# Optimization experiments

Hardware: AMD Instinct MI355X
Metric: run time of the kernel (lower is better)

## Reference

```python
import jax, jax.numpy as jnp
import numpy as np

B, R, DIM = 4096, 64, 128


def setup_inputs() -> dict:
    key = jax.random.key(0)
    ks = jax.random.split(key, 8)
    return {
        "query_emb": jax.random.normal(ks[0], (B, DIM), jnp.float32),
        "offset_emb": jax.random.normal(ks[1], (B, DIM), jnp.float32),
        "refer_embs": jax.random.normal(ks[2], (B, R, DIM), jnp.float32),
        "query_r": jax.random.normal(ks[3], (B, DIM), jnp.float32),
        "refer_r": jax.random.normal(ks[4], (B, R, DIM), jnp.float32),
        "start_embs": jax.random.normal(ks[5], (B, R, DIM), jnp.float32),
        # attn_layer_1: Linear(2*dim, dim); xavier-uniform-like scale
        "W1": jax.random.uniform(ks[6], (DIM, 2 * DIM), jnp.float32, -0.125, 0.125),
        "b1": jnp.zeros((DIM,), jnp.float32),
        # attn_layer_2: Linear(dim, dim)
        "W2": jax.random.uniform(ks[7], (DIM, DIM), jnp.float32, -0.125, 0.125),
        "b2": jnp.zeros((DIM,), jnp.float32),
    }


def reference(query_emb, offset_emb, refer_embs, query_r, refer_r, start_embs, W1, b1, W2, b2):
    # bias term per neighbor: [B, R, dim]
    bias = refer_embs - (start_embs + refer_r)
    # concat([refer_r, broadcast(query_r)]) @ W1.T split to avoid materializing the concat:
    # W1 = [W1_a | W1_b] over the 2*dim input axis
    W1a, W1b = W1[:, :DIM], W1[:, DIM:]
    h = jnp.einsum('brd,kd->brk', refer_r, W1a) \
        + jnp.einsum('bd,kd->bk', query_r, W1b)[:, None, :] + b1
    h = jax.nn.relu(h)  # [B, R, dim]
    attn = jnp.einsum('brk,dk->brd', h, W2) + b2  # attn_layer_2
    final_refer_emb = jnp.sum(attn * bias, axis=-2)  # [B, dim]
    final_query_emb = query_emb + final_refer_emb
    return (final_query_emb, offset_emb)
```

## Files before the change

### kernel.cpp

```cpp
#include <hip/hip_runtime.h>
#include <hip/hip_bf16.h>
#include <stdint.h>

#define BTOT 4096
#define RR   64
#define DIMD 128

typedef short s16x8 __attribute__((ext_vector_type(8)));
typedef float f32x4 __attribute__((ext_vector_type(4)));

__device__ __forceinline__ unsigned short f2bf(float x) {
  __hip_bfloat16 h = __float2bfloat16(x);
  return __builtin_bit_cast(unsigned short, h);
}
__device__ __forceinline__ float bf2f(unsigned short u) {
  unsigned int v = ((unsigned int)u) << 16;
  return __builtin_bit_cast(float, v);
}

__global__ __launch_bounds__(256) void prep_kernel(
    const float* __restrict__ W1, const float* __restrict__ b1,
    const float* __restrict__ query_r, const float* __restrict__ W2,
    const float* __restrict__ offset_emb,
    float* __restrict__ qproj, unsigned short* __restrict__ w1a_swz,
    unsigned short* __restrict__ w2_swz, float* __restrict__ out)
{
  __shared__ float w1b[128 * 132];
  __shared__ float qrs[256];
  const int tid = threadIdx.x;

  {
    const size_t ob = (size_t)blockIdx.x * 8 * DIMD + (size_t)tid * 4;
    *reinterpret_cast<float4*>(out + (size_t)BTOT * DIMD + ob) =
        *reinterpret_cast<const float4*>(offset_emb + ob);
  }
  {
    const int k = tid >> 1, d0 = (tid & 1) * 64;
    const float* src = W1 + k * 256 + 128 + d0;
    float* dst = &w1b[k * 132 + d0];
    #pragma unroll
    for (int i = 0; i < 64; i += 4)
      *reinterpret_cast<float4*>(dst + i) = *reinterpret_cast<const float4*>(src + i);
  }
  if (blockIdx.x < 2) {
    const float* Wsrc = (blockIdx.x == 0) ? W1 : W2;
    unsigned short* dstw = (blockIdx.x == 0) ? w1a_swz : w2_swz;
    const int stride = (blockIdx.x == 0) ? 256 : 128;
    for (int i = tid; i < 128 * 128; i += 256) {
      const int k = i >> 7, d = i & 127;
      dstw[k * 128 + (d ^ ((k & 7) << 3))] = f2bf(Wsrc[k * stride + d]);
    }
  }
  __syncthreads();

  const int b0 = blockIdx.x * 8;
  const int k = tid & 127, bh = tid >> 7;
  for (int p = 0; p < 4; ++p) {
    const int b = b0 + p * 2;
    qrs[tid] = query_r[(size_t)(b + bh) * DIMD + k];
    __syncthreads();
    float acc = b1[k];
    const float* qq = &qrs[bh * 128];
    const float* wr = &w1b[k * 132];
    #pragma unroll
    for (int d = 0; d < 128; d += 4) {
      float4 wv = *reinterpret_cast<const float4*>(wr + d);
      float4 qv = *reinterpret_cast<const float4*>(qq + d);
      acc = fmaf(wv.x, qv.x, acc); acc = fmaf(wv.y, qv.y, acc);
      acc = fmaf(wv.z, qv.z, acc); acc = fmaf(wv.w, qv.w, acc);
    }
    qproj[(size_t)(b + bh) * DIMD + k] = acc;
    __syncthreads();
  }
}

__global__ __launch_bounds__(512) void main_kernel(
    const float* __restrict__ query_emb,
    const float* __restrict__ refer_embs, const float* __restrict__ refer_r,
    const float* __restrict__ start_embs, const float* __restrict__ b2,
    const float* __restrict__ qproj, const unsigned short* __restrict__ w1a_swz,
    const unsigned short* __restrict__ w2_swz, float* __restrict__ out)
{
  __shared__ unsigned short lds_w1a[128 * 128];
  __shared__ unsigned short lds_w2[128 * 128];
  __shared__ unsigned short wbuf[8][16 * 64];

  const int tid  = threadIdx.x;
  const int wave = tid >> 6;
  const int lane = tid & 63;
  const int g    = lane >> 4;
  const int c    = lane & 15;

  {
    const uint4* s1 = reinterpret_cast<const uint4*>(w1a_swz);
    const uint4* s2 = reinterpret_cast<const uint4*>(w2_swz);
    uint4* d1 = reinterpret_cast<uint4*>(lds_w1a);
    uint4* d2 = reinterpret_cast<uint4*>(lds_w2);
    #pragma unroll
    for (int i = 0; i < 4; ++i) {
      d1[tid + 512 * i] = s1[tid + 512 * i];
      d2[tid + 512 * i] = s2[tid + 512 * i];
    }
  }
  __syncthreads();

  unsigned short* mybuf = &wbuf[wave][0];
  const int srl  = lane >> 2;
  const int q    = lane & 3;
  const int sw_s = (srl & 7) << 3;
  const int swc  = (c & 7) << 3;
  const int rl4  = 4 * g;

  const int b = blockIdx.x * 8 + wave;

  float qn[8], b2v[8], acc[8];
  #pragma unroll
  for (int nt = 0; nt < 8; ++nt) {
    qn[nt]  = qproj[(size_t)b * DIMD + nt * 16 + c];
    b2v[nt] = b2[nt * 16 + c];
    acc[nt] = 0.f;
  }

  for (int it = 0; it < 4; ++it) {
    const size_t rowbase = ((size_t)b * RR + it * 16 + srl) * DIMD;
    uint4 bp[4];
    f32x4 Ch[8];
    #pragma unroll
    for (int nt = 0; nt < 8; ++nt) Ch[nt] = (f32x4){qn[nt], qn[nt], qn[nt], qn[nt]};

    #pragma unroll
    for (int H = 0; H < 2; ++H) {
      const size_t gb = rowbase + H * 64 + q * 16;
      float4 rv[4], ev[4], sv[4];
      #pragma unroll
      for (int i = 0; i < 4; ++i) {
        rv[i] = *reinterpret_cast<const float4*>(refer_r    + gb + 4 * i);
        ev[i] = *reinterpret_cast<const float4*>(refer_embs + gb + 4 * i);
        sv[i] = *reinterpret_cast<const float4*>(start_embs + gb + 4 * i);
      }
      {
        unsigned short* wrow = &mybuf[srl * 64];
        #pragma unroll
        for (int gi = 0; gi < 2; ++gi) {
          union { unsigned short u[8]; uint4 v; } pk;
          const float4 a = rv[2 * gi], bq = rv[2 * gi + 1];
          pk.u[0] = f2bf(a.x);  pk.u[1] = f2bf(a.y);
          pk.u[2] = f2bf(a.z);  pk.u[3] = f2bf(a.w);
          pk.u[4] = f2bf(bq.x); pk.u[5] = f2bf(bq.y);
          pk.u[6] = f2bf(bq.z); pk.u[7] = f2bf(bq.w);
          *reinterpret_cast<uint4*>(&wrow[(q * 16 + gi * 8) ^ sw_s]) = pk.v;
        }
      }
      #pragma unroll
      for (int gi = 0; gi < 2; ++gi) {
        union { unsigned short u[8]; uint4 v; } pk;
        const float4 e0 = ev[2 * gi], s0 = sv[2 * gi], f0 = rv[2 * gi];
        const float4 e1 = ev[2 * gi + 1], s1 = sv[2 * gi + 1], f1 = rv[2 * gi + 1];
        pk.u[0] = f2bf(e0.x - s0.x - f0.x); pk.u[1] = f2bf(e0.y - s0.y - f0.y);
        pk.u[2] = f2bf(e0.z - s0.z - f0.z); pk.u[3] = f2bf(e0.w - s0.w - f0.w);
        pk.u[4] = f2bf(e1.x - s1.x - f1.x); pk.u[5] = f2bf(e1.y - s1.y - f1.y);
        pk.u[6] = f2bf(e1.z - s1.z - f1.z); pk.u[7] = f2bf(e1.w - s1.w - f1.w);
        bp[2 * H + gi] = pk.v;
      }
      asm volatile("s_waitcnt lgkmcnt(0)" ::: "memory");
      s16x8 af0 = *reinterpret_cast<const s16x8*>(&mybuf[c * 64 + ((g * 8) ^ swc)]);
      s16x8 af1 = *reinterpret_cast<const s16x8*>(&mybuf[c * 64 + ((32 + g * 8) ^ swc)]);
      #pragma unroll
      for (int ks2 = 0; ks2 < 2; ++ks2)
        #pragma unroll
        for (int nt = 0; nt < 8; ++nt) {
          s16x8 wf = *reinterpret_cast<const s16x8*>(
              &lds_w1a[(nt * 16 + c) * DIMD + ((H * 64 + ks2 * 32 + g * 8) ^ swc)]);
          Ch[nt] = __builtin_amdgcn_mfma_f32_16x16x32_bf16(ks2 ? af1 : af0, wf, Ch[nt], 0, 0, 0);
        }
      asm volatile("s_waitcnt lgkmcnt(0)" ::: "memory");
    }

    f32x4 Ca[8];
    #pragma unroll
    for (int nt = 0; nt < 8; ++nt) Ca[nt] = (f32x4){b2v[nt], b2v[nt], b2v[nt], b2v[nt]};
    #pragma unroll
    for (int H = 0; H < 2; ++H) {
      #pragma unroll
      for (int ntl = 0; ntl < 4; ++ntl)
        #pragma unroll
        for (int r = 0; r < 4; ++r) {
          const int rl = rl4 + r;
          mybuf[rl * 64 + ((ntl * 16 + c) ^ ((rl & 7) << 3))] =
              f2bf(fmaxf(Ch[4 * H + ntl][r], 0.f));
        }
      asm volatile("s_waitcnt lgkmcnt(0)" ::: "memory");
      s16x8 hf0 = *reinterpret_cast<const s16x8*>(&mybuf[c * 64 + ((g * 8) ^ swc)]);
      s16x8 hf1 = *reinterpret_cast<const s16x8*>(&mybuf[c * 64 + ((32 + g * 8) ^ swc)]);
      #pragma unroll
      for (int ks2 = 0; ks2 < 2; ++ks2)
        #pragma unroll
        for (int nt = 0; nt < 8; ++nt) {
          s16x8 wf = *reinterpret_cast<const s16x8*>(
              &lds_w2[(nt * 16 + c) * DIMD + ((H * 64 + ks2 * 32 + g * 8) ^ swc)]);
          Ca[nt] = __builtin_amdgcn_mfma_f32_16x16x32_bf16(ks2 ? hf1 : hf0, wf, Ca[nt], 0, 0, 0);
        }
      asm volatile("s_waitcnt lgkmcnt(0)" ::: "memory");
    }

    #pragma unroll
    for (int H = 0; H < 2; ++H) {
      {
        unsigned short* wrow = &mybuf[srl * 64];
        *reinterpret_cast<uint4*>(&wrow[(q * 16 + 0) ^ sw_s]) = bp[2 * H];
        *reinterpret_cast<uint4*>(&wrow[(q * 16 + 8) ^ sw_s]) = bp[2 * H + 1];
      }
      asm volatile("s_waitcnt lgkmcnt(0)" ::: "memory");
      #pragma unroll
      for (int ntl = 0; ntl < 4; ++ntl) {
        const int nt = 4 * H + ntl;
        float s = 0.f;
        #pragma unroll
        for (int r = 0; r < 4; ++r) {
          const int rl = rl4 + r;
          const float bcv = bf2f(mybuf[rl * 64 + ((ntl * 16 + c) ^ ((rl & 7) << 3))]);
          s = fmaf(Ca[nt][r], bcv, s);
        }
        s += __shfl_xor(s, 16);
        s += __shfl_xor(s, 32);
        acc[nt] += s;
      }
      asm volatile("s_waitcnt lgkmcnt(0)" ::: "memory");
    }
  }

  if (lane < 16) {
    #pragma unroll
    for (int nt = 0; nt < 8; ++nt)
      out[(size_t)b * DIMD + nt * 16 + c] =
          query_emb[(size_t)b * DIMD + nt * 16 + c] + acc[nt];
  }
}

extern "C" void kernel_launch(void* const* d_in, const int* in_sizes, int n_in,
                              void* d_out, int out_size, void* d_ws, size_t ws_size,
                              hipStream_t stream) {
  const float* query_emb  = (const float*)d_in[0];
  const float* offset_emb = (const float*)d_in[1];
  const float* refer_embs = (const float*)d_in[2];
  const float* query_r    = (const float*)d_in[3];
  const float* refer_r    = (const float*)d_in[4];
  const float* start_embs = (const float*)d_in[5];
  const float* W1 = (const float*)d_in[6];
  const float* b1 = (const float*)d_in[7];
  const float* W2 = (const float*)d_in[8];
  const float* b2 = (const float*)d_in[9];
  float* out = (float*)d_out;

  float* qproj = (float*)d_ws;
  unsigned short* w1a_swz =
      (unsigned short*)((char*)d_ws + (size_t)BTOT * DIMD * sizeof(float));
  unsigned short* w2_swz = w1a_swz + 128 * 128;

  hipLaunchKernelGGL(prep_kernel, dim3(512), dim3(256), 0, stream,
                     W1, b1, query_r, W2, offset_emb, qproj, w1a_swz, w2_swz, out);
  hipLaunchKernelGGL(main_kernel, dim3(512), dim3(512), 0, stream,
                     query_emb, refer_embs, refer_r, start_embs,
                     b2, qproj, w1a_swz, w2_swz, out);
}
```

Baseline: 109.9 us.

## Process full 128-wide rows per iteration with separate LDS tiles for relation and bias

Each iteration now issues all 24 float4 global loads for a 16-row tile at once, instead of two half-row phases. The bf16 relation tile and the bias tile are staged into separate per-wave LDS buffers that span the full 128 columns. This lets both MFMA chains run over K=128 without intermediate phases, and the inline s_waitcnt barriers are dropped. The aim is more memory-level parallelism and fewer LDS round-trips and waits. In exchange, LDS per block grows from about 80KB to 128KB, which likely cuts resident blocks per CU from two to one, and the larger load batch raises register pressure.

```diff
diff --git a/kernel.cpp b/kernel.cpp
--- a/kernel.cpp
+++ b/kernel.cpp
@@ -83,7 +83,8 @@
 {
   __shared__ unsigned short lds_w1a[128 * 128];
   __shared__ unsigned short lds_w2[128 * 128];
-  __shared__ unsigned short wbuf[8][16 * 64];
+  __shared__ unsigned short tbuf[8][16 * 128];
+  __shared__ unsigned short bbuf[8][16 * 128];
 
   const int tid  = threadIdx.x;
   const int wave = tid >> 6;
@@ -104,9 +105,10 @@
   }
   __syncthreads();
 
-  unsigned short* mybuf = &wbuf[wave][0];
+  unsigned short* myt = &tbuf[wave][0];
+  unsigned short* myb = &bbuf[wave][0];
   const int srl  = lane >> 2;
-  const int q    = lane & 3;
+  const int sd0  = (lane & 3) * 32;
   const int sw_s = (srl & 7) << 3;
   const int swc  = (c & 7) << 3;
   const int rl4  = 4 * g;
@@ -122,110 +124,90 @@
   }
 
   for (int it = 0; it < 4; ++it) {
-    const size_t rowbase = ((size_t)b * RR + it * 16 + srl) * DIMD;
-    uint4 bp[4];
+    const size_t gb = ((size_t)b * RR + it * 16 + srl) * DIMD + sd0;
+
+    float4 rv[8], ev[8], sv[8];
+    #pragma unroll
+    for (int i = 0; i < 8; ++i) rv[i] = *reinterpret_cast<const float4*>(refer_r    + gb + 4 * i);
+    #pragma unroll
+    for (int i = 0; i < 8; ++i) ev[i] = *reinterpret_cast<const float4*>(refer_embs + gb + 4 * i);
+    #pragma unroll
+    for (int i = 0; i < 8; ++i) sv[i] = *reinterpret_cast<const float4*>(start_embs + gb + 4 * i);
+
+    #pragma unroll
+    for (int gi = 0; gi < 4; ++gi) {
+      union { unsigned short u[8]; uint4 v; } pk;
+      const float4 a = rv[2 * gi], bq = rv[2 * gi + 1];
+      pk.u[0] = f2bf(a.x);  pk.u[1] = f2bf(a.y);
+      pk.u[2] = f2bf(a.z);  pk.u[3] = f2bf(a.w);
+      pk.u[4] = f2bf(bq.x); pk.u[5] = f2bf(bq.y);
+      pk.u[6] = f2bf(bq.z); pk.u[7] = f2bf(bq.w);
+      *reinterpret_cast<uint4*>(&myt[srl * DIMD + ((sd0 + gi * 8) ^ sw_s)]) = pk.v;
+    }
+    #pragma unroll
+    for (int gi = 0; gi < 4; ++gi) {
+      union { unsigned short u[8]; uint4 v; } pk;
+      const float4 e0 = ev[2 * gi], s0 = sv[2 * gi], f0 = rv[2 * gi];
+      const float4 e1 = ev[2 * gi + 1], s1 = sv[2 * gi + 1], f1 = rv[2 * gi + 1];
+      pk.u[0] = f2bf(e0.x - s0.x - f0.x); pk.u[1] = f2bf(e0.y - s0.y - f0.y);
+      pk.u[2] = f2bf(e0.z - s0.z - f0.z); pk.u[3] = f2bf(e0.w - s0.w - f0.w);
+      pk.u[4] = f2bf(e1.x - s1.x - f1.x); pk.u[5] = f2bf(e1.y - s1.y - f1.y);
+      pk.u[6] = f2bf(e1.z - s1.z - f1.z); pk.u[7] = f2bf(e1.w - s1.w - f1.w);
+      *reinterpret_cast<uint4*>(&myb[srl * DIMD + ((sd0 + gi * 8) ^ sw_s)]) = pk.v;
+    }
+
+    s16x8 af[4];
+    #pragma unroll
+    for (int ks = 0; ks < 4; ++ks)
+      af[ks] = *reinterpret_cast<const s16x8*>(&myt[c * DIMD + ((ks * 32 + g * 8) ^ swc)]);
     f32x4 Ch[8];
     #pragma unroll
     for (int nt = 0; nt < 8; ++nt) Ch[nt] = (f32x4){qn[nt], qn[nt], qn[nt], qn[nt]};
-
-    #pragma unroll
-    for (int H = 0; H < 2; ++H) {
-      const size_t gb = rowbase + H * 64 + q * 16;
-      float4 rv[4], ev[4], sv[4];
-      #pragma unroll
-      for (int i = 0; i < 4; ++i) {
-        rv[i] = *reinterpret_cast<const float4*>(refer_r    + gb + 4 * i);
-        ev[i] = *reinterpret_cast<const float4*>(refer_embs + gb + 4 * i);
-        sv[i] = *reinterpret_cast<const float4*>(start_embs + gb + 4 * i);
-      }
-      {
-        unsigned short* wrow = &mybuf[srl * 64];
-        #pragma unroll
-        for (int gi = 0; gi < 2; ++gi) {
-          union { unsigned short u[8]; uint4 v; } pk;
-          const float4 a = rv[2 * gi], bq = rv[2 * gi + 1];
-          pk.u[0] = f2bf(a.x);  pk.u[1] = f2bf(a.y);
-          pk.u[2] = f2bf(a.z);  pk.u[3] = f2bf(a.w);
-          pk.u[4] = f2bf(bq.x); pk.u[5] = f2bf(bq.y);
-          pk.u[6] = f2bf(bq.z); pk.u[7] = f2bf(bq.w);
-          *reinterpret_cast<uint4*>(&wrow[(q * 16 + gi * 8) ^ sw_s]) = pk.v;
-        }
-      }
-      #pragma unroll
-      for (int gi = 0; gi < 2; ++gi) {
-        union { unsigned short u[8]; uint4 v; } pk;
-        const float4 e0 = ev[2 * gi], s0 = sv[2 * gi], f0 = rv[2 * gi];
-        const float4 e1 = ev[2 * gi + 1], s1 = sv[2 * gi + 1], f1 = rv[2 * gi + 1];
-        pk.u[0] = f2bf(e0.x - s0.x - f0.x); pk.u[1] = f2bf(e0.y - s0.y - f0.y);
-        pk.u[2] = f2bf(e0.z - s0.z - f0.z); pk.u[3] = f2bf(e0.w - s0.w - f0.w);
-        pk.u[4] = f2bf(e1.x - s1.x - f1.x); pk.u[5] = f2bf(e1.y - s1.y - f1.y);
-        pk.u[6] = f2bf(e1.z - s1.z - f1.z); pk.u[7] = f2bf(e1.w - s1.w - f1.w);
-        bp[2 * H + gi] = pk.v;
-      }
-      asm volatile("s_waitcnt lgkmcnt(0)" ::: "memory");
-      s16x8 af0 = *reinterpret_cast<const s16x8*>(&mybuf[c * 64 + ((g * 8) ^ swc)]);
-      s16x8 af1 = *reinterpret_cast<const s16x8*>(&mybuf[c * 64 + ((32 + g * 8) ^ swc)]);
-      #pragma unroll
-      for (int ks2 = 0; ks2 < 2; ++ks2)
-        #pragma unroll
-        for (int nt = 0; nt < 8; ++nt) {
-          s16x8 wf = *reinterpret_cast<const s16x8*>(
-              &lds_w1a[(nt * 16 + c) * DIMD + ((H * 64 + ks2 * 32 + g * 8) ^ swc)]);
-          Ch[nt] = __builtin_amdgcn_mfma_f32_16x16x32_bf16(ks2 ? af1 : af0, wf, Ch[nt], 0, 0, 0);
-        }
-      asm volatile("s_waitcnt lgkmcnt(0)" ::: "memory");
-    }
-
+    #pragma unroll
+    for (int ks = 0; ks < 4; ++ks)
+      #pragma unroll
+      for (int nt = 0; nt < 8; ++nt) {
+        s16x8 wf = *reinterpret_cast<const s16x8*>(
+            &lds_w1a[(nt * 16 + c) * DIMD + ((ks * 32 + g * 8) ^ swc)]);
+        Ch[nt] = __builtin_amdgcn_mfma_f32_16x16x32_bf16(af[ks], wf, Ch[nt], 0, 0, 0);
+      }
+
+    #pragma unroll
+    for (int nt = 0; nt < 8; ++nt)
+      #pragma unroll
+      for (int r = 0; r < 4; ++r) {
+        const int rl = rl4 + r;
+        myt[rl * DIMD + ((nt * 16 + c) ^ ((rl & 7) << 3))] = f2bf(fmaxf(Ch[nt][r], 0.f));
+      }
+
+    s16x8 hf[4];
+    #pragma unroll
+    for (int ks = 0; ks < 4; ++ks)
+      hf[ks] = *reinterpret_cast<const s16x8*>(&myt[c * DIMD + ((ks * 32 + g * 8) ^ swc)]);
     f32x4 Ca[8];
     #pragma unroll
     for (int nt = 0; nt < 8; ++nt) Ca[nt] = (f32x4){b2v[nt], b2v[nt], b2v[nt], b2v[nt]};
     #pragma unroll
-    for (int H = 0; H < 2; ++H) {
-      #pragma unroll
-      for (int ntl = 0; ntl < 4; ++ntl)
-        #pragma unroll
-        for (int r = 0; r < 4; ++r) {
-          const int rl = rl4 + r;
-          mybuf[rl * 64 + ((ntl * 16 + c) ^ ((rl & 7) << 3))] =
-              f2bf(fmaxf(Ch[4 * H + ntl][r], 0.f));
-        }
-      asm volatile("s_waitcnt lgkmcnt(0)" ::: "memory");
-      s16x8 hf0 = *reinterpret_cast<const s16x8*>(&mybuf[c * 64 + ((g * 8) ^ swc)]);
-      s16x8 hf1 = *reinterpret_cast<const s16x8*>(&mybuf[c * 64 + ((32 + g * 8) ^ swc)]);
-      #pragma unroll
-      for (int ks2 = 0; ks2 < 2; ++ks2)
-        #pragma unroll
-        for (int nt = 0; nt < 8; ++nt) {
-          s16x8 wf = *reinterpret_cast<const s16x8*>(
-              &lds_w2[(nt * 16 + c) * DIMD + ((H * 64 + ks2 * 32 + g * 8) ^ swc)]);
-          Ca[nt] = __builtin_amdgcn_mfma_f32_16x16x32_bf16(ks2 ? hf1 : hf0, wf, Ca[nt], 0, 0, 0);
-        }
-      asm volatile("s_waitcnt lgkmcnt(0)" ::: "memory");
-    }
-
-    #pragma unroll
-    for (int H = 0; H < 2; ++H) {
-      {
-        unsigned short* wrow = &mybuf[srl * 64];
-        *reinterpret_cast<uint4*>(&wrow[(q * 16 + 0) ^ sw_s]) = bp[2 * H];
-        *reinterpret_cast<uint4*>(&wrow[(q * 16 + 8) ^ sw_s]) = bp[2 * H + 1];
-      }
-      asm volatile("s_waitcnt lgkmcnt(0)" ::: "memory");
-      #pragma unroll
-      for (int ntl = 0; ntl < 4; ++ntl) {
-        const int nt = 4 * H + ntl;
-        float s = 0.f;
-        #pragma unroll
-        for (int r = 0; r < 4; ++r) {
-          const int rl = rl4 + r;
-          const float bcv = bf2f(mybuf[rl * 64 + ((ntl * 16 + c) ^ ((rl & 7) << 3))]);
-          s = fmaf(Ca[nt][r], bcv, s);
-        }
-        s += __shfl_xor(s, 16);
-        s += __shfl_xor(s, 32);
-        acc[nt] += s;
-      }
-      asm volatile("s_waitcnt lgkmcnt(0)" ::: "memory");
+    for (int ks = 0; ks < 4; ++ks)
+      #pragma unroll
+      for (int nt = 0; nt < 8; ++nt) {
+        s16x8 wf = *reinterpret_cast<const s16x8*>(
+            &lds_w2[(nt * 16 + c) * DIMD + ((ks * 32 + g * 8) ^ swc)]);
+        Ca[nt] = __builtin_amdgcn_mfma_f32_16x16x32_bf16(hf[ks], wf, Ca[nt], 0, 0, 0);
+      }
+
+    #pragma unroll
+    for (int nt = 0; nt < 8; ++nt) {
+      float s = 0.f;
+      #pragma unroll
+      for (int r = 0; r < 4; ++r) {
+        const int rl = rl4 + r;
+        const float bcv = bf2f(myb[rl * DIMD + ((nt * 16 + c) ^ ((rl & 7) << 3))]);
+        s = fmaf(Ca[nt][r], bcv, s);
+      }
+      s += __shfl_xor(s, 16);
+      s += __shfl_xor(s, 32);
+      acc[nt] += s;
     }
   }
 
```

Measured after the change: 146.1 us. 1.33x slower.
